# Kernel optimization log

Measured on AMD Instinct MI355X. Metric: run time of the kernel, lower is better.

The kernel has to match this reference:

```python
import jax, jax.numpy as jnp
import numpy as np

B, N, C = 8, 4096, 768
H = 4 * C  # mlp hidden
EPS = 1e-7
LN_EPS = 1e-5


def _ln(x, g, b):
    mu = jnp.mean(x, axis=-1, keepdims=True)
    var = jnp.mean((x - mu) ** 2, axis=-1, keepdims=True)
    return (x - mu) * jax.lax.rsqrt(var + LN_EPS) * g + b


def _mlp(z, w1, b1, w2, b2):
    return jax.nn.gelu(z @ w1 + b1, approximate=False) @ w2 + b2


def setup_inputs() -> dict:
    key = jax.random.key(0)
    ks = jax.random.split(key, 16)
    s = 1.0 / np.sqrt(C)
    inp = {
        "x": jax.random.normal(ks[0], (B, N, C), jnp.float32),
        "y": jax.random.normal(ks[1], (B, N, C), jnp.float32),
        "mask": jax.random.randint(ks[2], (B, N, 1), 0, 2).astype(jnp.float32),
        "h": 64,
        "w": 64,
        "ln1_g": jnp.ones((C,), jnp.float32),
        "ln1_b": jnp.zeros((C,), jnp.float32),
        "Wq": jax.random.normal(ks[3], (C, C), jnp.float32) * s,
        "Wk": jax.random.normal(ks[4], (C, C), jnp.float32) * s,
        "Wv": jax.random.normal(ks[5], (C, C), jnp.float32) * s,
        "Wpx": jax.random.normal(ks[6], (2 * C, C), jnp.float32) * s,
        "Wpy": jax.random.normal(ks[7], (2 * C, C), jnp.float32) * s,
        "ln2_g": jnp.ones((C,), jnp.float32),
        "ln2_b": jnp.zeros((C,), jnp.float32),
        "fx1_w": jax.random.normal(ks[8], (C, H), jnp.float32) * s,
        "fx1_b": jnp.zeros((H,), jnp.float32),
        "fx2_w": jax.random.normal(ks[9], (H, C), jnp.float32) / np.sqrt(H),
        "fx2_b": jnp.zeros((C,), jnp.float32),
        "fy1_w": jax.random.normal(ks[10], (C, H), jnp.float32) * s,
        "fy1_b": jnp.zeros((H,), jnp.float32),
        "fy2_w": jax.random.normal(ks[11], (H, C), jnp.float32) / np.sqrt(H),
        "fy2_b": jnp.zeros((C,), jnp.float32),
    }
    return inp


def _minmax(s):
    mn = jnp.min(s, axis=1, keepdims=True)
    mx = jnp.max(s, axis=1, keepdims=True)
    return (s - mn) / (mx - mn + EPS)


def reference(x, y, mask, h, w, ln1_g, ln1_b, Wq, Wk, Wv, Wpx, Wpy,
              ln2_g, ln2_b, fx1_w, fx1_b, fx2_w, fx2_b, fy1_w, fy1_b, fy2_w, fy2_b):
    b, n, c = x.shape
    m = mask.reshape(b, n, 1)  # binary mask per token
    xn = _ln(x, ln1_g, ln1_b)
    yn = _ln(y, ln1_g, ln1_b)
    q = yn @ Wq  # (b,n,c)
    k = xn @ Wk
    v = xn @ Wv
    # masked GAP pools (Weighted_GAP): (b,c)
    fg = jnp.sum(q * m, axis=1) / (jnp.sum(m, axis=1) + 5e-4)
    bg = jnp.sum(q * (1.0 - m), axis=1) / (jnp.sum(1.0 - m, axis=1) + 5e-4)
    k_nrm = jnp.linalg.norm(k, axis=2)  # (b,n)
    fg_nrm = jnp.linalg.norm(fg, axis=1, keepdims=True)  # (b,1)
    bg_nrm = jnp.linalg.norm(bg, axis=1, keepdims=True)
    fg_s = jnp.einsum('bnc,bc->bn', k, fg) / (k_nrm * fg_nrm + EPS)
    bg_s = jnp.einsum('bnc,bc->bn', k, bg) / (k_nrm * bg_nrm + EPS)
    scores = _minmax(fg_s) - _minmax(bg_s)  # (b,n)
    pseudo_mask = scores.reshape(b, 1, h, w)
    attn = jax.nn.softmax(jnp.where(scores < 0, scores - 100.0, scores), axis=1)
    query_pro = jnp.einsum('bn,bnc->bc', attn, v)  # (b,c)
    qp_nrm = jnp.linalg.norm(query_pro, axis=1, keepdims=True)
    sim = jnp.sum(query_pro * fg, axis=1, keepdims=True) / (qp_nrm * fg_nrm + EPS)
    sim = (sim + 1.0) * 0.5  # (b,1)
    pro = sim * fg + (1.0 - sim) * query_pro  # (b,c)
    pro_b = jnp.broadcast_to(pro[:, None, :], x.shape)
    xo = x + jnp.concatenate([x, pro_b], axis=-1) @ Wpx
    yo = y + jnp.concatenate([y, pro_b], axis=-1) @ Wpy
    xo = xo + _mlp(_ln(xo, ln2_g, ln2_b), fx1_w, fx1_b, fx2_w, fx2_b)
    yo = yo + _mlp(_ln(yo, ln2_g, ln2_b), fy1_w, fy1_b, fy2_w, fy2_b)
    return (xo, yo, pseudo_mask)
```

## Files before the change

### kernel.cpp

```cpp
#include <hip/hip_runtime.h>
#include <math.h>

#define B_ 8
#define N_ 4096
#define C_ 768
#define H_ 3072
#define M_ (B_*N_)
#define NSPLIT 16

typedef unsigned short u16;
typedef unsigned int u32;
typedef __attribute__((ext_vector_type(8))) __bf16 bf16x8;
typedef __attribute__((ext_vector_type(4))) float f32x4;
typedef __attribute__((ext_vector_type(4))) unsigned short u16x4;

__device__ __forceinline__ u16 f2bf(float f){
  u32 u = __float_as_uint(f);
  u32 r = (u + 0x7FFFu + ((u >> 16) & 1u)) >> 16;
  return (u16)r;
}
__device__ __forceinline__ float bf2f(u16 h){
  return __uint_as_float(((u32)h) << 16);
}
__device__ __forceinline__ void gload_lds16(const void* g, void* l){
  __builtin_amdgcn_global_load_lds((const __attribute__((address_space(1))) void*)g,
                                   (__attribute__((address_space(3))) void*)l, 16, 0, 0);
}

template<int EPI>
__global__ __launch_bounds__(256) void gemm_bf16(
    const u16* __restrict__ A, const u16* __restrict__ BT,
    int K, int N, int NBN,
    void* __restrict__ outp,
    const float* __restrict__ resid,
    const float* __restrict__ rowv,
    const float* __restrict__ bias)
{
  __shared__ u16 lds[2][8192];
  const int tid = threadIdx.x;
  const int wid = tid >> 6, lane = tid & 63;

  const int nwg = gridDim.x;
  int wg = blockIdx.x;
  wg = (wg & 7) * (nwg >> 3) + (wg >> 3);
  const int GMN = 8 * NBN;
  const int g = wg / GMN, r = wg % GMN;
  const int bm = (g*8 + (r & 7)) * 128;
  const int bn = (r >> 3) * 128;

  const int wr = wid >> 1, wc = wid & 1;

  f32x4 acc[4][4];
#pragma unroll
  for (int i=0;i<4;i++)
#pragma unroll
    for (int j=0;j<4;j++) acc[i][j] = (f32x4){0.f,0.f,0.f,0.f};

  const int idx0 = tid, idx1 = tid + 256;
  const u16* agp0 = A  + (size_t)(bm + (idx0>>2))*K + (idx0&3)*8;
  const u16* agp1 = A  + (size_t)(bm + (idx1>>2))*K + (idx1&3)*8;
  const u16* bgp0 = BT + (size_t)(bn + (idx0>>2))*K + (idx0&3)*8;
  const u16* bgp1 = BT + (size_t)(bn + (idx1>>2))*K + (idx1&3)*8;

  auto STAGE = [&](int c){
    u16* base = lds[c];
    gload_lds16(agp0, base + wid*512);
    gload_lds16(agp1, base + 2048 + wid*512);
    gload_lds16(bgp0, base + 4096 + wid*512);
    gload_lds16(bgp1, base + 6144 + wid*512);
    agp0 += 32; agp1 += 32; bgp0 += 32; bgp1 += 32;
  };

  const int aoff = (wr*64 + (lane&15))*32 + (lane>>4)*8;
  const int boff = 4096 + (wc*64 + (lane&15))*32 + (lane>>4)*8;

  const int nk = K >> 5;
  STAGE(0);
  __syncthreads();
  int cur = 0;
  for (int kk=0; kk<nk; kk++){
    if (kk+1 < nk) STAGE(cur^1);
    bf16x8 av[4], bv[4];
    const u16* pa = &lds[cur][aoff];
    const u16* pb = &lds[cur][boff];
#pragma unroll
    for (int i=0;i<4;i++){
      av[i] = *reinterpret_cast<const bf16x8*>(pa + i*512);
      bv[i] = *reinterpret_cast<const bf16x8*>(pb + i*512);
    }
#pragma unroll
    for (int i=0;i<4;i++)
#pragma unroll
      for (int j=0;j<4;j++)
        acc[i][j] = __builtin_amdgcn_mfma_f32_16x16x32_bf16(av[i], bv[j], acc[i][j], 0, 0, 0);
    __syncthreads();
    cur ^= 1;
  }

  const int col0 = bn + wc*64 + (lane & 15);
  const int row0 = bm + wr*64 + ((lane >> 4) << 2);
#pragma unroll
  for (int i=0;i<4;i++){
#pragma unroll
    for (int j=0;j<4;j++){
#pragma unroll
      for (int r2=0;r2<4;r2++){
        const int row = row0 + i*16 + r2;
        const int cj  = col0 + j*16;
        const size_t o = (size_t)row*N + cj;
        const float va = acc[i][j][r2];
        if constexpr (EPI == 0){
          ((u16*)outp)[o] = f2bf(va);
        } else if constexpr (EPI == 1){
          ((float*)outp)[o] = resid[o] + va + rowv[(row >> 12)*N + cj];
        } else if constexpr (EPI == 2){
          const float z = va + bias[cj];
          ((u16*)outp)[o] = f2bf(0.5f*z*(1.0f + erff(z*0.70710678f)));
        } else {
          float* po = (float*)outp + o;
          *po += va + bias[cj];
        }
      }
    }
  }
}

__global__ __launch_bounds__(256) void ln_fwd(const float* __restrict__ in,
    const float* __restrict__ gam, const float* __restrict__ bet,
    u16* __restrict__ out)
{
  const int row  = blockIdx.x*4 + (threadIdx.x >> 6);
  const int lane = threadIdx.x & 63;
  const float* p = in + (size_t)row * C_;
  float4 v0 = *reinterpret_cast<const float4*>(p + lane*4);
  float4 v1 = *reinterpret_cast<const float4*>(p + lane*4 + 256);
  float4 v2 = *reinterpret_cast<const float4*>(p + lane*4 + 512);
  float s  = v0.x+v0.y+v0.z+v0.w + v1.x+v1.y+v1.z+v1.w + v2.x+v2.y+v2.z+v2.w;
  float sq = v0.x*v0.x+v0.y*v0.y+v0.z*v0.z+v0.w*v0.w
           + v1.x*v1.x+v1.y*v1.y+v1.z*v1.z+v1.w*v1.w
           + v2.x*v2.x+v2.y*v2.y+v2.z*v2.z+v2.w*v2.w;
#pragma unroll
  for (int o=32;o>0;o>>=1){ s += __shfl_xor(s,o); sq += __shfl_xor(sq,o); }
  const float mu = s * (1.f/C_);
  const float rs = rsqrtf(sq*(1.f/C_) - mu*mu + 1e-5f);
  float4 g0 = *reinterpret_cast<const float4*>(gam + lane*4);
  float4 g1 = *reinterpret_cast<const float4*>(gam + lane*4 + 256);
  float4 g2 = *reinterpret_cast<const float4*>(gam + lane*4 + 512);
  float4 b0 = *reinterpret_cast<const float4*>(bet + lane*4);
  float4 b1 = *reinterpret_cast<const float4*>(bet + lane*4 + 256);
  float4 b2 = *reinterpret_cast<const float4*>(bet + lane*4 + 512);
  u16* op = out + (size_t)row * C_;
  u16x4 o0, o1, o2;
  o0[0]=f2bf((v0.x-mu)*rs*g0.x+b0.x); o0[1]=f2bf((v0.y-mu)*rs*g0.y+b0.y);
  o0[2]=f2bf((v0.z-mu)*rs*g0.z+b0.z); o0[3]=f2bf((v0.w-mu)*rs*g0.w+b0.w);
  o1[0]=f2bf((v1.x-mu)*rs*g1.x+b1.x); o1[1]=f2bf((v1.y-mu)*rs*g1.y+b1.y);
  o1[2]=f2bf((v1.z-mu)*rs*g1.z+b1.z); o1[3]=f2bf((v1.w-mu)*rs*g1.w+b1.w);
  o2[0]=f2bf((v2.x-mu)*rs*g2.x+b2.x); o2[1]=f2bf((v2.y-mu)*rs*g2.y+b2.y);
  o2[2]=f2bf((v2.z-mu)*rs*g2.z+b2.z); o2[3]=f2bf((v2.w-mu)*rs*g2.w+b2.w);
  *reinterpret_cast<u16x4*>(op + lane*4)       = o0;
  *reinterpret_cast<u16x4*>(op + lane*4 + 256) = o1;
  *reinterpret_cast<u16x4*>(op + lane*4 + 512) = o2;
}

__global__ __launch_bounds__(256) void cvt_bf16(const float* __restrict__ in,
                                                u16* __restrict__ out, int n4)
{
  int i = blockIdx.x*256 + threadIdx.x;
  if (i < n4){
    float4 v = reinterpret_cast<const float4*>(in)[i];
    u16x4 o; o[0]=f2bf(v.x); o[1]=f2bf(v.y); o[2]=f2bf(v.z); o[3]=f2bf(v.w);
    *reinterpret_cast<u16x4*>(out + (size_t)i*4) = o;
  }
}

__global__ __launch_bounds__(256) void transpose_cvt(const float* __restrict__ in,
    u16* __restrict__ out, int R, int Cc)
{
  __shared__ float tile[32][33];
  const int c0 = blockIdx.x*32, r0 = blockIdx.y*32;
  const int tx = threadIdx.x & 31, ty = threadIdx.x >> 5;
#pragma unroll
  for (int i=0;i<32;i+=8)
    tile[ty+i][tx] = in[(size_t)(r0+ty+i)*Cc + c0+tx];
  __syncthreads();
#pragma unroll
  for (int i=0;i<32;i+=8)
    out[(size_t)(c0+ty+i)*R + r0+tx] = f2bf(tile[tx][ty+i]);
}

__global__ __launch_bounds__(256) void msum_kernel(const float* __restrict__ mask,
                                                   float* __restrict__ msum)
{
  __shared__ float sm[4];
  const int b = blockIdx.x;
  float s = 0.f;
  for (int i=threadIdx.x;i<N_;i+=256) s += mask[(size_t)b*N_+i];
#pragma unroll
  for (int o=32;o>0;o>>=1) s += __shfl_down(s,o);
  if ((threadIdx.x&63)==0) sm[threadIdx.x>>6]=s;
  __syncthreads();
  if (threadIdx.x==0) msum[b] = sm[0]+sm[1]+sm[2]+sm[3];
}

__global__ __launch_bounds__(256) void pool_partial(const u16* __restrict__ q,
    const float* __restrict__ mask, float* __restrict__ pm, float* __restrict__ pa)
{
  const int c = blockIdx.x*256 + threadIdx.x;
  const int b = blockIdx.y, z = blockIdx.z;
  const int n0 = z*(N_/NSPLIT);
  const u16* qp = q + ((size_t)b*N_ + n0)*C_ + c;
  const float* mp = mask + (size_t)b*N_ + n0;
  float am=0.f, aa=0.f;
  for (int n=0;n<N_/NSPLIT;n++){
    float v = bf2f(qp[(size_t)n*C_]);
    float m = mp[n];
    am += v*m; aa += v;
  }
  const size_t o = ((size_t)z*B_ + b)*C_ + c;
  pm[o]=am; pa[o]=aa;
}

__global__ __launch_bounds__(256) void pool_final(const float* __restrict__ pm,
    const float* __restrict__ pa, const float* __restrict__ msum,
    float* __restrict__ fg, float* __restrict__ bg)
{
  const int c = blockIdx.x*256 + threadIdx.x;
  const int b = blockIdx.y;
  float s_m=0.f, s_a=0.f;
  for (int z=0;z<NSPLIT;z++){ size_t o=((size_t)z*B_+b)*C_+c; s_m+=pm[o]; s_a+=pa[o]; }
  const float ms = msum[b];
  fg[b*C_+c] = s_m/(ms + 5e-4f);
  bg[b*C_+c] = (s_a - s_m)/((float)N_ - ms + 5e-4f);
}

__global__ __launch_bounds__(256) void norm_kernel(const float* __restrict__ fg,
    const float* __restrict__ bg, float* __restrict__ fgn, float* __restrict__ bgn)
{
  __shared__ float sm[8];
  const int b = blockIdx.x;
  float f=0.f, g=0.f;
  for (int i=threadIdx.x;i<C_;i+=256){
    float a=fg[b*C_+i]; f+=a*a;
    float c=bg[b*C_+i]; g+=c*c;
  }
#pragma unroll
  for (int o=32;o>0;o>>=1){ f+=__shfl_down(f,o); g+=__shfl_down(g,o); }
  if ((threadIdx.x&63)==0){ sm[threadIdx.x>>6]=f; sm[4+(threadIdx.x>>6)]=g; }
  __syncthreads();
  if (threadIdx.x==0){
    fgn[b]=sqrtf(sm[0]+sm[1]+sm[2]+sm[3]);
    bgn[b]=sqrtf(sm[4]+sm[5]+sm[6]+sm[7]);
  }
}

__global__ __launch_bounds__(256) void score_kernel(const u16* __restrict__ k,
    const float* __restrict__ fg, const float* __restrict__ bg,
    const float* __restrict__ fgn, const float* __restrict__ bgn,
    float* __restrict__ fg_s, float* __restrict__ bg_s)
{
  __shared__ float sm[12];
  const int t = blockIdx.x;
  const int b = t >> 12;
  const u16* kp = k + (size_t)t*C_;
  float df=0.f, db=0.f, kk=0.f;
  for (int i=threadIdx.x;i<C_;i+=256){
    float kv = bf2f(kp[i]);
    df += kv*fg[b*C_+i]; db += kv*bg[b*C_+i]; kk += kv*kv;
  }
#pragma unroll
  for (int o=32;o>0;o>>=1){ df+=__shfl_down(df,o); db+=__shfl_down(db,o); kk+=__shfl_down(kk,o); }
  const int wid = threadIdx.x>>6;
  if ((threadIdx.x&63)==0){ sm[wid]=df; sm[4+wid]=db; sm[8+wid]=kk; }
  __syncthreads();
  if (threadIdx.x==0){
    df=sm[0]+sm[1]+sm[2]+sm[3]; db=sm[4]+sm[5]+sm[6]+sm[7]; kk=sm[8]+sm[9]+sm[10]+sm[11];
    const float kn = sqrtf(kk);
    fg_s[t] = df/(kn*fgn[b]+1e-7f);
    bg_s[t] = db/(kn*bgn[b]+1e-7f);
  }
}

__global__ __launch_bounds__(256) void minmax_kernel(const float* __restrict__ fg_s,
    const float* __restrict__ bg_s, float* __restrict__ mm)
{
  __shared__ float sm[16];
  const int b = blockIdx.x;
  float mnf=1e30f, mxf=-1e30f, mnb=1e30f, mxb=-1e30f;
  for (int i=threadIdx.x;i<N_;i+=256){
    float a = fg_s[(size_t)b*N_+i]; mnf=fminf(mnf,a); mxf=fmaxf(mxf,a);
    float c = bg_s[(size_t)b*N_+i]; mnb=fminf(mnb,c); mxb=fmaxf(mxb,c);
  }
#pragma unroll
  for (int o=32;o>0;o>>=1){
    mnf=fminf(mnf,__shfl_down(mnf,o)); mxf=fmaxf(mxf,__shfl_down(mxf,o));
    mnb=fminf(mnb,__shfl_down(mnb,o)); mxb=fmaxf(mxb,__shfl_down(mxb,o));
  }
  const int wid = threadIdx.x>>6;
  if ((threadIdx.x&63)==0){ sm[wid]=mnf; sm[4+wid]=mxf; sm[8+wid]=mnb; sm[12+wid]=mxb; }
  __syncthreads();
  if (threadIdx.x==0){
    mm[b*4+0]=fminf(fminf(sm[0],sm[1]),fminf(sm[2],sm[3]));
    mm[b*4+1]=fmaxf(fmaxf(sm[4],sm[5]),fmaxf(sm[6],sm[7]));
    mm[b*4+2]=fminf(fminf(sm[8],sm[9]),fminf(sm[10],sm[11]));
    mm[b*4+3]=fmaxf(fmaxf(sm[12],sm[13]),fmaxf(sm[14],sm[15]));
  }
}

__global__ __launch_bounds__(256) void scorefin_kernel(const float* __restrict__ fg_s,
    const float* __restrict__ bg_s, const float* __restrict__ mm,
    float* __restrict__ pseudo, float* __restrict__ escr, float* __restrict__ epart)
{
  __shared__ float sm[4];
  const int b = blockIdx.y, z = blockIdx.x;
  const int t = z*256 + threadIdx.x;
  const size_t o = (size_t)b*N_ + t;
  const float mnf=mm[b*4+0], mxf=mm[b*4+1], mnb=mm[b*4+2], mxb=mm[b*4+3];
  const float s = (fg_s[o]-mnf)/(mxf-mnf+1e-7f) - (bg_s[o]-mnb)/(mxb-mnb+1e-7f);
  pseudo[o] = s;
  const float e = expf(s < 0.f ? s - 100.f : s);
  escr[o] = e;
  float ps = e;
#pragma unroll
  for (int off=32;off>0;off>>=1) ps += __shfl_down(ps,off);
  if ((threadIdx.x&63)==0) sm[threadIdx.x>>6]=ps;
  __syncthreads();
  if (threadIdx.x==0) epart[b*16+z] = sm[0]+sm[1]+sm[2]+sm[3];
}

__global__ void denom_kernel(const float* __restrict__ epart, float* __restrict__ denom){
  const int b = threadIdx.x;
  if (b < B_){ float s=0.f; for (int z=0;z<16;z++) s+=epart[b*16+z]; denom[b]=s; }
}

__global__ __launch_bounds__(256) void vsum_partial(const u16* __restrict__ v,
    const float* __restrict__ e, float* __restrict__ pv)
{
  const int c = blockIdx.x*256 + threadIdx.x;
  const int b = blockIdx.y, z = blockIdx.z;
  const int n0 = z*(N_/NSPLIT);
  const u16* vp = v + ((size_t)b*N_ + n0)*C_ + c;
  const float* ep = e + (size_t)b*N_ + n0;
  float acc=0.f;
  for (int n=0;n<N_/NSPLIT;n++) acc += bf2f(vp[(size_t)n*C_])*ep[n];
  pv[((size_t)z*B_+b)*C_+c] = acc;
}

__global__ __launch_bounds__(256) void vsum_final(const float* __restrict__ pv,
    const float* __restrict__ denom, float* __restrict__ qp)
{
  const int c = blockIdx.x*256 + threadIdx.x;
  const int b = blockIdx.y;
  float s=0.f;
  for (int z=0;z<NSPLIT;z++) s += pv[((size_t)z*B_+b)*C_+c];
  qp[b*C_+c] = s/denom[b];
}

__global__ __launch_bounds__(256) void pro_kernel(const float* __restrict__ qp,
    const float* __restrict__ fg, const float* __restrict__ fgn, float* __restrict__ pro)
{
  __shared__ float sm[8];
  __shared__ float simsh;
  const int b = blockIdx.x;
  float d=0.f, qq=0.f;
  for (int i=threadIdx.x;i<C_;i+=256){ float a=qp[b*C_+i]; d+=a*fg[b*C_+i]; qq+=a*a; }
#pragma unroll
  for (int o=32;o>0;o>>=1){ d+=__shfl_down(d,o); qq+=__shfl_down(qq,o); }
  if ((threadIdx.x&63)==0){ sm[threadIdx.x>>6]=d; sm[4+(threadIdx.x>>6)]=qq; }
  __syncthreads();
  if (threadIdx.x==0){
    d=sm[0]+sm[1]+sm[2]+sm[3]; qq=sm[4]+sm[5]+sm[6]+sm[7];
    simsh = (d/(sqrtf(qq)*fgn[b]+1e-7f)+1.f)*0.5f;
  }
  __syncthreads();
  const float sim = simsh;
  for (int i=threadIdx.x;i<C_;i+=256)
    pro[b*C_+i] = sim*fg[b*C_+i] + (1.f-sim)*qp[b*C_+i];
}

__global__ __launch_bounds__(256) void rowvec_kernel(const float* __restrict__ pro,
    const float* __restrict__ Wp, float* __restrict__ row)
{
  const int j = blockIdx.x*256 + threadIdx.x;
  const int b = blockIdx.y;
  const float* w = Wp + (size_t)C_*C_ + j;
  const float* p = pro + b*C_;
  float acc=0.f;
#pragma unroll 4
  for (int c=0;c<C_;c++) acc += p[c]*w[(size_t)c*C_];
  row[b*C_+j] = acc;
}

extern "C" void kernel_launch(void* const* d_in, const int* in_sizes, int n_in,
                              void* d_out, int out_size, void* d_ws, size_t ws_size,
                              hipStream_t stream)
{
  const float* x     = (const float*)d_in[0];
  const float* y     = (const float*)d_in[1];
  const float* mask  = (const float*)d_in[2];
  const float* ln1_g = (const float*)d_in[5];
  const float* ln1_b = (const float*)d_in[6];
  const float* Wq    = (const float*)d_in[7];
  const float* Wk    = (const float*)d_in[8];
  const float* Wv    = (const float*)d_in[9];
  const float* Wpx   = (const float*)d_in[10];
  const float* Wpy   = (const float*)d_in[11];
  const float* ln2_g = (const float*)d_in[12];
  const float* ln2_b = (const float*)d_in[13];
  const float* fx1_w = (const float*)d_in[14];
  const float* fx1_b = (const float*)d_in[15];
  const float* fx2_w = (const float*)d_in[16];
  const float* fx2_b = (const float*)d_in[17];
  const float* fy1_w = (const float*)d_in[18];
  const float* fy1_b = (const float*)d_in[19];
  const float* fy2_w = (const float*)d_in[20];
  const float* fy2_b = (const float*)d_in[21];

  float* out    = (float*)d_out;
  float* out_xo = out;
  float* out_yo = out + (size_t)M_*C_;
  float* out_ps = out + 2*(size_t)M_*C_;

  char* ws = (char*)d_ws;
  const size_t ACT = (size_t)M_*C_;
  u16* R0  = (u16*)ws;
  u16* xnb = R0;
  u16* ynb = R0 + ACT;
  u16* kb  = R0 + 2*ACT;
  u16* vb  = R0 + 3*ACT;
  u16* hid = R0;
  u16* qb  = (u16*)(ws + 4*ACT*2);
  u16* wp  = (u16*)(ws + 5*ACT*2);
  u16* WqT  = wp;
  u16* WkT  = wp + 1*589824;
  u16* WvT  = wp + 2*589824;
  u16* WpxT = wp + 3*589824;
  u16* WpyT = wp + 4*589824;
  u16* fx1T = wp + 5*589824;
  u16* fx2T = fx1T + 2359296;
  u16* fy1T = fx2T + 2359296;
  u16* fy2T = fy1T + 2359296;
  float* st   = (float*)(ws + 5*ACT*2 + 24772608);
  float* msum = st;
  float* fgn  = st + 8;
  float* bgn  = st + 16;
  float* denom= st + 24;
  float* mm   = st + 32;
  float* fg   = st + 64;
  float* bg   = st + 6208;
  float* qp   = st + 12352;
  float* pro  = st + 18496;
  float* rowx = st + 24640;
  float* rowy = st + 30784;
  float* epart= st + 36928;
  float* fg_s = st + 37056;
  float* bg_s = st + 69824;
  float* escr = st + 102592;
  float* pm   = st + 135360;
  float* pa   = st + 233664;
  float* pv   = st + 331968;

  dim3 tb(256);

  transpose_cvt<<<dim3(24,24),tb,0,stream>>>(Wq,  WqT,  C_, C_);
  transpose_cvt<<<dim3(24,24),tb,0,stream>>>(Wk,  WkT,  C_, C_);
  transpose_cvt<<<dim3(24,24),tb,0,stream>>>(Wv,  WvT,  C_, C_);
  transpose_cvt<<<dim3(24,24),tb,0,stream>>>(Wpx, WpxT, C_, C_);
  transpose_cvt<<<dim3(24,24),tb,0,stream>>>(Wpy, WpyT, C_, C_);
  transpose_cvt<<<dim3(96,24),tb,0,stream>>>(fx1_w, fx1T, C_, H_);
  transpose_cvt<<<dim3(24,96),tb,0,stream>>>(fx2_w, fx2T, H_, C_);
  transpose_cvt<<<dim3(96,24),tb,0,stream>>>(fy1_w, fy1T, C_, H_);
  transpose_cvt<<<dim3(24,96),tb,0,stream>>>(fy2_w, fy2T, H_, C_);

  ln_fwd<<<M_/4,tb,0,stream>>>(x, ln1_g, ln1_b, xnb);
  ln_fwd<<<M_/4,tb,0,stream>>>(y, ln1_g, ln1_b, ynb);

  gemm_bf16<0><<<dim3(256*6),tb,0,stream>>>(ynb, WqT, C_, C_, 6, qb, nullptr,nullptr,nullptr);
  gemm_bf16<0><<<dim3(256*6),tb,0,stream>>>(xnb, WkT, C_, C_, 6, kb, nullptr,nullptr,nullptr);
  gemm_bf16<0><<<dim3(256*6),tb,0,stream>>>(xnb, WvT, C_, C_, 6, vb, nullptr,nullptr,nullptr);

  msum_kernel<<<B_,tb,0,stream>>>(mask, msum);
  pool_partial<<<dim3(3,B_,NSPLIT),tb,0,stream>>>(qb, mask, pm, pa);
  pool_final<<<dim3(3,B_),tb,0,stream>>>(pm, pa, msum, fg, bg);
  norm_kernel<<<B_,tb,0,stream>>>(fg, bg, fgn, bgn);
  score_kernel<<<M_,tb,0,stream>>>(kb, fg, bg, fgn, bgn, fg_s, bg_s);
  minmax_kernel<<<B_,tb,0,stream>>>(fg_s, bg_s, mm);
  scorefin_kernel<<<dim3(16,B_),tb,0,stream>>>(fg_s, bg_s, mm, out_ps, escr, epart);
  denom_kernel<<<1,64,0,stream>>>(epart, denom);
  vsum_partial<<<dim3(3,B_,NSPLIT),tb,0,stream>>>(vb, escr, pv);
  vsum_final<<<dim3(3,B_),tb,0,stream>>>(pv, denom, qp);
  pro_kernel<<<B_,tb,0,stream>>>(qp, fg, fgn, pro);
  rowvec_kernel<<<dim3(3,B_),tb,0,stream>>>(pro, Wpx, rowx);
  rowvec_kernel<<<dim3(3,B_),tb,0,stream>>>(pro, Wpy, rowy);

  cvt_bf16<<<(ACT/4+255)/256,tb,0,stream>>>(x, xnb, (int)(ACT/4));
  cvt_bf16<<<(ACT/4+255)/256,tb,0,stream>>>(y, ynb, (int)(ACT/4));

  gemm_bf16<1><<<dim3(256*6),tb,0,stream>>>(xnb, WpxT, C_, C_, 6, out_xo, x, rowx, nullptr);
  gemm_bf16<1><<<dim3(256*6),tb,0,stream>>>(ynb, WpyT, C_, C_, 6, out_yo, y, rowy, nullptr);

  ln_fwd<<<M_/4,tb,0,stream>>>(out_xo, ln2_g, ln2_b, qb);
  gemm_bf16<2><<<dim3(256*24),tb,0,stream>>>(qb, fx1T, C_, H_, 24, hid, nullptr,nullptr, fx1_b);
  gemm_bf16<3><<<dim3(256*6),tb,0,stream>>>(hid, fx2T, H_, C_, 6, out_xo, nullptr,nullptr, fx2_b);

  ln_fwd<<<M_/4,tb,0,stream>>>(out_yo, ln2_g, ln2_b, qb);
  gemm_bf16<2><<<dim3(256*24),tb,0,stream>>>(qb, fy1T, C_, H_, 24, hid, nullptr,nullptr, fy1_b);
  gemm_bf16<3><<<dim3(256*6),tb,0,stream>>>(hid, fy2T, H_, C_, 6, out_yo, nullptr,nullptr, fy2_b);
}
```

Baseline: 1.803 ms.

## Replace GEMM with 256x256-tile 8-wave kernel using swizzled LDS and phased pipeline

Replaces the 128x128 tile, 4-wave bf16 GEMM with a 256x256 tile, 8-wave kernel that stages 64-wide K chunks into 128KB of double-buffered LDS through direct global-to-LDS loads. LDS columns are XOR-swizzled to avoid bank conflicts. The main loop is split into hand-scheduled phases using sched_barrier, setprio and explicit vmcnt/lgkmcnt waits so loads overlap the MFMA work. The goal is more operand reuse per byte loaded and better latency hiding. The cost is 128KB of LDS per block, which limits occupancy, and fragile manual synchronisation.

```diff
diff --git a/kernel.cpp b/kernel.cpp
--- a/kernel.cpp
+++ b/kernel.cpp
@@ -27,88 +27,131 @@
                                    (__attribute__((address_space(3))) void*)l, 16, 0, 0);
 }
 
+
+#define MM4(FM, AV) \
+  acc[FM][0] = __builtin_amdgcn_mfma_f32_16x16x32_bf16(AV, b0, acc[FM][0],0,0,0); \
+  acc[FM][1] = __builtin_amdgcn_mfma_f32_16x16x32_bf16(AV, b1, acc[FM][1],0,0,0); \
+  acc[FM][2] = __builtin_amdgcn_mfma_f32_16x16x32_bf16(AV, b2, acc[FM][2],0,0,0); \
+  acc[FM][3] = __builtin_amdgcn_mfma_f32_16x16x32_bf16(AV, b3, acc[FM][3],0,0,0);
+
+#define STAGE(H2) do { if ((H2) < Htot){                                     \
+  const int kt_ = (H2)>>2, ty_ = (H2)&3;                                     \
+  const int kh_ = ty_>>1; const int isA_ = ty_&1;                            \
+  const size_t ko_ = (size_t)kt_*64 + (size_t)kh_*32;                        \
+  char* ld_ = ldsc + ((kt_&1)<<16) + ((isA_^1)<<15) + (kh_<<14) + tid*16;    \
+  const u16* g0_ = (isA_ ? Ap + Ab0 : Bp + Bb0) + ko_;                       \
+  const u16* g1_ = (isA_ ? Ap + Ab1 : Bp + Bb1) + ko_;                       \
+  gload_lds16(g0_, ld_);                                                     \
+  gload_lds16(g1_, ld_ + 8192);                                              \
+}} while(0)
+
+#define PHASE(BUFB, KHB, FMQ, LOADB, VMN) do {                               \
+  __builtin_amdgcn_sched_barrier(0);                                         \
+  const u16* pa_ = ldsu + (((BUFB)+(KHB))>>1) + aoffA;                       \
+  bf16x8 a0_ = *(const bf16x8*)(pa_ + ((FMQ)*4+0)*512);                      \
+  bf16x8 a1_ = *(const bf16x8*)(pa_ + ((FMQ)*4+1)*512);                      \
+  bf16x8 a2_ = *(const bf16x8*)(pa_ + ((FMQ)*4+2)*512);                      \
+  bf16x8 a3_ = *(const bf16x8*)(pa_ + ((FMQ)*4+3)*512);                      \
+  if (LOADB){                                                                \
+    const u16* pb_ = ldsu + (((BUFB)+32768+(KHB))>>1) + boffB;               \
+    b0 = *(const bf16x8*)(pb_ + 0*512);                                      \
+    b1 = *(const bf16x8*)(pb_ + 1*512);                                      \
+    b2 = *(const bf16x8*)(pb_ + 2*512);                                      \
+    b3 = *(const bf16x8*)(pb_ + 3*512);                                      \
+  }                                                                          \
+  STAGE(hh); hh++;                                                           \
+  __builtin_amdgcn_sched_barrier(0);                                         \
+  __builtin_amdgcn_s_barrier();                                              \
+  asm volatile("s_waitcnt lgkmcnt(0)" ::: "memory");                         \
+  __builtin_amdgcn_sched_barrier(0);                                         \
+  __builtin_amdgcn_s_setprio(1);                                             \
+  MM4((FMQ)*4+0, a0_)                                                        \
+  MM4((FMQ)*4+1, a1_)                                                        \
+  MM4((FMQ)*4+2, a2_)                                                        \
+  MM4((FMQ)*4+3, a3_)                                                        \
+  __builtin_amdgcn_s_setprio(0);                                             \
+  if ((VMN) == 6) { asm volatile("s_waitcnt vmcnt(6)" ::: "memory"); }       \
+  else if ((VMN) == 0) { asm volatile("s_waitcnt vmcnt(0)" ::: "memory"); }  \
+  __builtin_amdgcn_s_barrier();                                              \
+} while(0)
+
 template<int EPI>
-__global__ __launch_bounds__(256) void gemm_bf16(
-    const u16* __restrict__ A, const u16* __restrict__ BT,
+__global__ __launch_bounds__(512, 2) void gemm256(
+    const u16* __restrict__ Ap, const u16* __restrict__ Bp,
     int K, int N, int NBN,
     void* __restrict__ outp,
     const float* __restrict__ resid,
     const float* __restrict__ rowv,
     const float* __restrict__ bias)
 {
-  __shared__ u16 lds[2][8192];
+  __shared__ __align__(16) char ldsraw[131072];
+  char* ldsc = ldsraw;
+  const u16* ldsu = (const u16*)ldsraw;
+
   const int tid = threadIdx.x;
   const int wid = tid >> 6, lane = tid & 63;
+  const int wr = wid >> 2, wc = wid & 3;
+  const int l15 = lane & 15;
 
   const int nwg = gridDim.x;
   int wg = blockIdx.x;
   wg = (wg & 7) * (nwg >> 3) + (wg >> 3);
-  const int GMN = 8 * NBN;
-  const int g = wg / GMN, r = wg % GMN;
-  const int bm = (g*8 + (r & 7)) * 128;
-  const int bn = (r >> 3) * 128;
-
-  const int wr = wid >> 1, wc = wid & 1;
-
-  f32x4 acc[4][4];
-#pragma unroll
-  for (int i=0;i<4;i++)
+  const int bm = (wg / NBN) * 256;
+  const int bn = (wg % NBN) * 256;
+
+  f32x4 acc[8][4];
+#pragma unroll
+  for (int i=0;i<8;i++)
 #pragma unroll
     for (int j=0;j<4;j++) acc[i][j] = (f32x4){0.f,0.f,0.f,0.f};
 
-  const int idx0 = tid, idx1 = tid + 256;
-  const u16* agp0 = A  + (size_t)(bm + (idx0>>2))*K + (idx0&3)*8;
-  const u16* agp1 = A  + (size_t)(bm + (idx1>>2))*K + (idx1&3)*8;
-  const u16* bgp0 = BT + (size_t)(bn + (idx0>>2))*K + (idx0&3)*8;
-  const u16* bgp1 = BT + (size_t)(bn + (idx1>>2))*K + (idx1&3)*8;
-
-  auto STAGE = [&](int c){
-    u16* base = lds[c];
-    gload_lds16(agp0, base + wid*512);
-    gload_lds16(agp1, base + 2048 + wid*512);
-    gload_lds16(bgp0, base + 4096 + wid*512);
-    gload_lds16(bgp1, base + 6144 + wid*512);
-    agp0 += 32; agp1 += 32; bgp0 += 32; bgp1 += 32;
-  };
-
-  const int aoff = (wr*64 + (lane&15))*32 + (lane>>4)*8;
-  const int boff = 4096 + (wc*64 + (lane&15))*32 + (lane>>4)*8;
-
-  const int nk = K >> 5;
-  STAGE(0);
-  __syncthreads();
-  int cur = 0;
-  for (int kk=0; kk<nk; kk++){
-    if (kk+1 < nk) STAGE(cur^1);
-    bf16x8 av[4], bv[4];
-    const u16* pa = &lds[cur][aoff];
-    const u16* pb = &lds[cur][boff];
-#pragma unroll
-    for (int i=0;i<4;i++){
-      av[i] = *reinterpret_cast<const bf16x8*>(pa + i*512);
-      bv[i] = *reinterpret_cast<const bf16x8*>(pb + i*512);
-    }
-#pragma unroll
-    for (int i=0;i<4;i++)
-#pragma unroll
-      for (int j=0;j<4;j++)
-        acc[i][j] = __builtin_amdgcn_mfma_f32_16x16x32_bf16(av[i], bv[j], acc[i][j], 0, 0, 0);
-    __syncthreads();
-    cur ^= 1;
-  }
-
-  const int col0 = bn + wc*64 + (lane & 15);
-  const int row0 = bm + wr*64 + ((lane >> 4) << 2);
-#pragma unroll
-  for (int i=0;i<4;i++){
-#pragma unroll
-    for (int j=0;j<4;j++){
-#pragma unroll
-      for (int r2=0;r2<4;r2++){
-        const int row = row0 + i*16 + r2;
-        const int cj  = col0 + j*16;
+  const int r0s = tid >> 2, c0s = (tid & 3) ^ ((tid >> 3) & 3);
+  const size_t Ab0 = (size_t)(bm + r0s)*K       + (size_t)c0s*8;
+  const size_t Ab1 = (size_t)(bm + 128 + r0s)*K + (size_t)c0s*8;
+  const size_t Bb0 = (size_t)(bn + r0s)*K       + (size_t)c0s*8;
+  const size_t Bb1 = (size_t)(bn + 128 + r0s)*K + (size_t)c0s*8;
+
+  const int physcb = ((lane >> 4) << 4) ^ (((l15 >> 1) & 3) << 4);
+  const int aoffA = (wr*128 + l15)*32 + (physcb >> 1);
+  const int boffB = (wc*64  + l15)*32 + (physcb >> 1);
+
+  const int T = K >> 6;
+  const int Htot = T*4;
+  bf16x8 b0, b1, b2, b3;
+
+  int hh = 0;
+  STAGE(0); STAGE(1); STAGE(2); STAGE(3);
+  asm volatile("s_waitcnt vmcnt(4)" ::: "memory");
+  STAGE(4); STAGE(5); STAGE(6);
+  asm volatile("s_waitcnt vmcnt(6)" ::: "memory");
+  __builtin_amdgcn_s_barrier();
+  hh = 7;
+
+  for (int kt = 0; kt < T; kt += 2){
+    const int vm4 = (kt+1 == T-1) ? 0 : 6;
+    const int vm8 = (kt+2 >= T) ? -1 : 6;
+    PHASE(0,     0,     0, 1, -1);
+    PHASE(0,     0,     1, 0, -1);
+    PHASE(0,     16384, 0, 1, -1);
+    PHASE(0,     16384, 1, 0, vm4);
+    PHASE(65536, 0,     0, 1, -1);
+    PHASE(65536, 0,     1, 0, -1);
+    PHASE(65536, 16384, 0, 1, -1);
+    PHASE(65536, 16384, 1, 0, vm8);
+  }
+
+  const int col0 = bn + wc*64 + l15;
+  const int row0 = bm + wr*128 + ((lane >> 4) << 2);
+#pragma unroll
+  for (int fm=0; fm<8; fm++){
+#pragma unroll
+    for (int fn=0; fn<4; fn++){
+#pragma unroll
+      for (int r2=0; r2<4; r2++){
+        const int row = row0 + fm*16 + r2;
+        const int cj  = col0 + fn*16;
         const size_t o = (size_t)row*N + cj;
-        const float va = acc[i][j][r2];
+        const float va = acc[fm][fn][r2];
         if constexpr (EPI == 0){
           ((u16*)outp)[o] = f2bf(va);
         } else if constexpr (EPI == 1){
@@ -460,6 +503,7 @@
   float* pv   = st + 331968;
 
   dim3 tb(256);
+  dim3 tg(512);
 
   transpose_cvt<<<dim3(24,24),tb,0,stream>>>(Wq,  WqT,  C_, C_);
   transpose_cvt<<<dim3(24,24),tb,0,stream>>>(Wk,  WkT,  C_, C_);
@@ -474,9 +518,9 @@
   ln_fwd<<<M_/4,tb,0,stream>>>(x, ln1_g, ln1_b, xnb);
   ln_fwd<<<M_/4,tb,0,stream>>>(y, ln1_g, ln1_b, ynb);
 
-  gemm_bf16<0><<<dim3(256*6),tb,0,stream>>>(ynb, WqT, C_, C_, 6, qb, nullptr,nullptr,nullptr);
-  gemm_bf16<0><<<dim3(256*6),tb,0,stream>>>(xnb, WkT, C_, C_, 6, kb, nullptr,nullptr,nullptr);
-  gemm_bf16<0><<<dim3(256*6),tb,0,stream>>>(xnb, WvT, C_, C_, 6, vb, nullptr,nullptr,nullptr);
+  gemm256<0><<<dim3(128*3),tg,0,stream>>>(ynb, WqT, C_, C_, 3, qb, nullptr,nullptr,nullptr);
+  gemm256<0><<<dim3(128*3),tg,0,stream>>>(xnb, WkT, C_, C_, 3, kb, nullptr,nullptr,nullptr);
+  gemm256<0><<<dim3(128*3),tg,0,stream>>>(xnb, WvT, C_, C_, 3, vb, nullptr,nullptr,nullptr);
 
   msum_kernel<<<B_,tb,0,stream>>>(mask, msum);
   pool_partial<<<dim3(3,B_,NSPLIT),tb,0,stream>>>(qb, mask, pm, pa);
@@ -495,14 +539,14 @@
   cvt_bf16<<<(ACT/4+255)/256,tb,0,stream>>>(x, xnb, (int)(ACT/4));
   cvt_bf16<<<(ACT/4+255)/256,tb,0,stream>>>(y, ynb, (int)(ACT/4));
 
-  gemm_bf16<1><<<dim3(256*6),tb,0,stream>>>(xnb, WpxT, C_, C_, 6, out_xo, x, rowx, nullptr);
-  gemm_bf16<1><<<dim3(256*6),tb,0,stream>>>(ynb, WpyT, C_, C_, 6, out_yo, y, rowy, nullptr);
+  gemm256<1><<<dim3(128*3),tg,0,stream>>>(xnb, WpxT, C_, C_, 3, out_xo, x, rowx, nullptr);
+  gemm256<1><<<dim3(128*3),tg,0,stream>>>(ynb, WpyT, C_, C_, 3, out_yo, y, rowy, nullptr);
 
   ln_fwd<<<M_/4,tb,0,stream>>>(out_xo, ln2_g, ln2_b, qb);
-  gemm_bf16<2><<<dim3(256*24),tb,0,stream>>>(qb, fx1T, C_, H_, 24, hid, nullptr,nullptr, fx1_b);
-  gemm_bf16<3><<<dim3(256*6),tb,0,stream>>>(hid, fx2T, H_, C_, 6, out_xo, nullptr,nullptr, fx2_b);
+  gemm256<2><<<dim3(128*12),tg,0,stream>>>(qb, fx1T, C_, H_, 12, hid, nullptr,nullptr, fx1_b);
+  gemm256<3><<<dim3(128*3),tg,0,stream>>>(hid, fx2T, H_, C_, 3, out_xo, nullptr,nullptr, fx2_b);
 
   ln_fwd<<<M_/4,tb,0,stream>>>(out_yo, ln2_g, ln2_b, qb);
-  gemm_bf16<2><<<dim3(256*24),tb,0,stream>>>(qb, fy1T, C_, H_, 24, hid, nullptr,nullptr, fy1_b);
-  gemm_bf16<3><<<dim3(256*6),tb,0,stream>>>(hid, fy2T, H_, C_, 6, out_yo, nullptr,nullptr, fy2_b);
-}
+  gemm256<2><<<dim3(128*12),tg,0,stream>>>(qb, fy1T, C_, H_, 12, hid, nullptr,nullptr, fy1_b);
+  gemm256<3><<<dim3(128*3),tg,0,stream>>>(hid, fy2T, H_, C_, 3, out_yo, nullptr,nullptr, fy2_b);
+}
```

Result: slower. 1.895 ms (+5.1%).

## Pool before projecting: replace Q and V GEMMs with pooled vector-matrix products

Applied to the files above, without the earlier changes.

By linearity, the masked pools of q equal the pooled normalized y multiplied by Wq, and the attention-weighted sum of v equals the weighted sum of normalized x multiplied by Wv. The full Q and V GEMMs over all tokens, along with their weight transposes, are replaced by pooling the bf16 LN outputs first and then running small per-batch vector-matrix kernels in fp32 on the original weights. This removes two large GEMMs and the associated activation traffic. Numerics shift slightly because the projection now happens after pooling in fp32 instead of on bf16 rounded products.

```diff
diff --git a/kernel.cpp b/kernel.cpp
--- a/kernel.cpp
+++ b/kernel.cpp
@@ -222,15 +222,43 @@
 
 __global__ __launch_bounds__(256) void pool_final(const float* __restrict__ pm,
     const float* __restrict__ pa, const float* __restrict__ msum,
-    float* __restrict__ fg, float* __restrict__ bg)
+    float* __restrict__ fgin, float* __restrict__ bgin)
 {
   const int c = blockIdx.x*256 + threadIdx.x;
   const int b = blockIdx.y;
   float s_m=0.f, s_a=0.f;
   for (int z=0;z<NSPLIT;z++){ size_t o=((size_t)z*B_+b)*C_+c; s_m+=pm[o]; s_a+=pa[o]; }
   const float ms = msum[b];
-  fg[b*C_+c] = s_m/(ms + 5e-4f);
-  bg[b*C_+c] = (s_a - s_m)/((float)N_ - ms + 5e-4f);
+  fgin[b*C_+c] = s_m/(ms + 5e-4f);
+  bgin[b*C_+c] = (s_a - s_m)/((float)N_ - ms + 5e-4f);
+}
+
+__global__ __launch_bounds__(256) void vecmat(const float* __restrict__ in,
+    const float* __restrict__ W, int rowoff, float* __restrict__ outv)
+{
+  const int j = blockIdx.x*256 + threadIdx.x;
+  const int b = blockIdx.y;
+  const float* w = W + (size_t)rowoff*C_ + j;
+  const float* p = in + b*C_;
+  float acc=0.f;
+#pragma unroll 4
+  for (int c=0;c<C_;c++) acc += p[c]*w[(size_t)c*C_];
+  outv[b*C_+j] = acc;
+}
+
+__global__ __launch_bounds__(256) void vecmat2(const float* __restrict__ in1,
+    const float* __restrict__ in2, const float* __restrict__ W,
+    float* __restrict__ o1, float* __restrict__ o2)
+{
+  const int j = blockIdx.x*256 + threadIdx.x;
+  const int b = blockIdx.y;
+  const float* w = W + j;
+  const float* p1 = in1 + b*C_;
+  const float* p2 = in2 + b*C_;
+  float a1=0.f, a2=0.f;
+#pragma unroll 4
+  for (int c=0;c<C_;c++){ float wv = w[(size_t)c*C_]; a1 += p1[c]*wv; a2 += p2[c]*wv; }
+  o1[b*C_+j]=a1; o2[b*C_+j]=a2;
 }
 
 __global__ __launch_bounds__(256) void norm_kernel(const float* __restrict__ fg,
@@ -332,27 +360,27 @@
   if (b < B_){ float s=0.f; for (int z=0;z<16;z++) s+=epart[b*16+z]; denom[b]=s; }
 }
 
-__global__ __launch_bounds__(256) void vsum_partial(const u16* __restrict__ v,
+__global__ __launch_bounds__(256) void vpool_partial(const u16* __restrict__ xn,
     const float* __restrict__ e, float* __restrict__ pv)
 {
   const int c = blockIdx.x*256 + threadIdx.x;
   const int b = blockIdx.y, z = blockIdx.z;
   const int n0 = z*(N_/NSPLIT);
-  const u16* vp = v + ((size_t)b*N_ + n0)*C_ + c;
+  const u16* vp = xn + ((size_t)b*N_ + n0)*C_ + c;
   const float* ep = e + (size_t)b*N_ + n0;
   float acc=0.f;
   for (int n=0;n<N_/NSPLIT;n++) acc += bf2f(vp[(size_t)n*C_])*ep[n];
   pv[((size_t)z*B_+b)*C_+c] = acc;
 }
 
-__global__ __launch_bounds__(256) void vsum_final(const float* __restrict__ pv,
-    const float* __restrict__ denom, float* __restrict__ qp)
+__global__ __launch_bounds__(256) void vpool_final(const float* __restrict__ pv,
+    const float* __restrict__ denom, float* __restrict__ vpin)
 {
   const int c = blockIdx.x*256 + threadIdx.x;
   const int b = blockIdx.y;
   float s=0.f;
   for (int z=0;z<NSPLIT;z++) s += pv[((size_t)z*B_+b)*C_+c];
-  qp[b*C_+c] = s/denom[b];
+  vpin[b*C_+c] = s/denom[b];
 }
 
 __global__ __launch_bounds__(256) void pro_kernel(const float* __restrict__ qp,
@@ -375,19 +403,6 @@
   const float sim = simsh;
   for (int i=threadIdx.x;i<C_;i+=256)
     pro[b*C_+i] = sim*fg[b*C_+i] + (1.f-sim)*qp[b*C_+i];
-}
-
-__global__ __launch_bounds__(256) void rowvec_kernel(const float* __restrict__ pro,
-    const float* __restrict__ Wp, float* __restrict__ row)
-{
-  const int j = blockIdx.x*256 + threadIdx.x;
-  const int b = blockIdx.y;
-  const float* w = Wp + (size_t)C_*C_ + j;
-  const float* p = pro + b*C_;
-  float acc=0.f;
-#pragma unroll 4
-  for (int c=0;c<C_;c++) acc += p[c]*w[(size_t)c*C_];
-  row[b*C_+j] = acc;
 }
 
 extern "C" void kernel_launch(void* const* d_in, const int* in_sizes, int n_in,
@@ -426,20 +441,17 @@
   u16* xnb = R0;
   u16* ynb = R0 + ACT;
   u16* kb  = R0 + 2*ACT;
-  u16* vb  = R0 + 3*ACT;
   u16* hid = R0;
   u16* qb  = (u16*)(ws + 4*ACT*2);
   u16* wp  = (u16*)(ws + 5*ACT*2);
-  u16* WqT  = wp;
-  u16* WkT  = wp + 1*589824;
-  u16* WvT  = wp + 2*589824;
-  u16* WpxT = wp + 3*589824;
-  u16* WpyT = wp + 4*589824;
-  u16* fx1T = wp + 5*589824;
+  u16* WkT  = wp;
+  u16* WpxT = wp + 1*589824;
+  u16* WpyT = wp + 2*589824;
+  u16* fx1T = wp + 3*589824;
   u16* fx2T = fx1T + 2359296;
   u16* fy1T = fx2T + 2359296;
   u16* fy2T = fy1T + 2359296;
-  float* st   = (float*)(ws + 5*ACT*2 + 24772608);
+  float* st   = (float*)(ws + 5*ACT*2 + (size_t)(3*589824 + 4*2359296)*2);
   float* msum = st;
   float* fgn  = st + 8;
   float* bgn  = st + 16;
@@ -458,12 +470,13 @@
   float* pm   = st + 135360;
   float* pa   = st + 233664;
   float* pv   = st + 331968;
+  float* fgin = st + 430272;
+  float* bgin = st + 436416;
+  float* vpin = st + 442560;
 
   dim3 tb(256);
 
-  transpose_cvt<<<dim3(24,24),tb,0,stream>>>(Wq,  WqT,  C_, C_);
   transpose_cvt<<<dim3(24,24),tb,0,stream>>>(Wk,  WkT,  C_, C_);
-  transpose_cvt<<<dim3(24,24),tb,0,stream>>>(Wv,  WvT,  C_, C_);
   transpose_cvt<<<dim3(24,24),tb,0,stream>>>(Wpx, WpxT, C_, C_);
   transpose_cvt<<<dim3(24,24),tb,0,stream>>>(Wpy, WpyT, C_, C_);
   transpose_cvt<<<dim3(96,24),tb,0,stream>>>(fx1_w, fx1T, C_, H_);
@@ -474,23 +487,26 @@
   ln_fwd<<<M_/4,tb,0,stream>>>(x, ln1_g, ln1_b, xnb);
   ln_fwd<<<M_/4,tb,0,stream>>>(y, ln1_g, ln1_b, ynb);
 
-  gemm_bf16<0><<<dim3(256*6),tb,0,stream>>>(ynb, WqT, C_, C_, 6, qb, nullptr,nullptr,nullptr);
   gemm_bf16<0><<<dim3(256*6),tb,0,stream>>>(xnb, WkT, C_, C_, 6, kb, nullptr,nullptr,nullptr);
-  gemm_bf16<0><<<dim3(256*6),tb,0,stream>>>(xnb, WvT, C_, C_, 6, vb, nullptr,nullptr,nullptr);
 
   msum_kernel<<<B_,tb,0,stream>>>(mask, msum);
-  pool_partial<<<dim3(3,B_,NSPLIT),tb,0,stream>>>(qb, mask, pm, pa);
-  pool_final<<<dim3(3,B_),tb,0,stream>>>(pm, pa, msum, fg, bg);
+  pool_partial<<<dim3(3,B_,NSPLIT),tb,0,stream>>>(ynb, mask, pm, pa);
+  pool_final<<<dim3(3,B_),tb,0,stream>>>(pm, pa, msum, fgin, bgin);
+  vecmat2<<<dim3(3,B_),tb,0,stream>>>(fgin, bgin, Wq, fg, bg);
   norm_kernel<<<B_,tb,0,stream>>>(fg, bg, fgn, bgn);
+
   score_kernel<<<M_,tb,0,stream>>>(kb, fg, bg, fgn, bgn, fg_s, bg_s);
   minmax_kernel<<<B_,tb,0,stream>>>(fg_s, bg_s, mm);
   scorefin_kernel<<<dim3(16,B_),tb,0,stream>>>(fg_s, bg_s, mm, out_ps, escr, epart);
   denom_kernel<<<1,64,0,stream>>>(epart, denom);
-  vsum_partial<<<dim3(3,B_,NSPLIT),tb,0,stream>>>(vb, escr, pv);
-  vsum_final<<<dim3(3,B_),tb,0,stream>>>(pv, denom, qp);
+
+  vpool_partial<<<dim3(3,B_,NSPLIT),tb,0,stream>>>(xnb, escr, pv);
+  vpool_final<<<dim3(3,B_),tb,0,stream>>>(pv, denom, vpin);
+  vecmat<<<dim3(3,B_),tb,0,stream>>>(vpin, Wv, 0, qp);
+
   pro_kernel<<<B_,tb,0,stream>>>(qp, fg, fgn, pro);
-  rowvec_kernel<<<dim3(3,B_),tb,0,stream>>>(pro, Wpx, rowx);
-  rowvec_kernel<<<dim3(3,B_),tb,0,stream>>>(pro, Wpy, rowy);
+  vecmat<<<dim3(3,B_),tb,0,stream>>>(pro, Wpx, C_, rowx);
+  vecmat<<<dim3(3,B_),tb,0,stream>>>(pro, Wpy, C_, rowy);
 
   cvt_bf16<<<(ACT/4+255)/256,tb,0,stream>>>(x, xnb, (int)(ACT/4));
   cvt_bf16<<<(ACT/4+255)/256,tb,0,stream>>>(y, ynb, (int)(ACT/4));
```

Result: slower. 1.866 ms (+3.5%).
